# Optimization experiments

Hardware: AMD Instinct MI355X
Metric: run time of the kernel (lower is better)

Reference implementation:

```python
import jax, jax.numpy as jnp
import numpy as np

V, E, H, L = 32000, 512, 512, 2


def _cell(x, h, c, Wih, Whh, bih, bhh):
    # PyTorch LSTM cell, gate order i,f,g,o
    g = x @ Wih.T + bih + h @ Whh.T + bhh
    i, f, gg, o = jnp.split(g, 4, axis=-1)
    c = jax.nn.sigmoid(f) * c + jax.nn.sigmoid(i) * jnp.tanh(gg)
    h = jax.nn.sigmoid(o) * jnp.tanh(c)
    return h, c


def _run_layer(x, p):
    # x: [B, S, in], scan over time
    B = x.shape[0]
    h0 = jnp.zeros((B, H), x.dtype)

    def step(carry, xt):
        h, c = carry
        h, c = _cell(xt, h, c, *p)
        return (h, c), h

    (hT, cT), hs = jax.lax.scan(step, (h0, h0), jnp.swapaxes(x, 0, 1))
    return jnp.swapaxes(hs, 0, 1), hT, cT


def _forward(xs, ys, emb, enc_p, dec_p, attn_W, comb_W):
    # ---- Encoder (2-layer unidirectional LSTM) ----
    x = emb[xs]                      # [B, Senc, E]
    hs, cs = [], []
    for l in range(L):
        x, hT, cT = _run_layer(x, enc_p[l])
        hs.append(hT)
        cs.append(cT)
    enc_out = x                      # [B, Senc, H] (top layer)
    h = jnp.stack(hs)                # [L, B, H]
    c = jnp.stack(cs)
    neg = (1.0 - (xs > 0).astype(enc_out.dtype)) * 1e20  # [B, Senc]
    emb_out = jax.lax.stop_gradient(emb)  # shared output weight is detached

    # ---- Decoder: per-timestep pre-attention ('general') + LSTM ----
    def step(carry, yt):
        h, c = carry
        xe = emb[yt]                              # [B, E]
        hid = h[-1] @ attn_W.T                    # [B, H]
        pw = jnp.einsum('bh,bsh->bs', hid, enc_out) - neg
        aw = jax.nn.softmax(pw, axis=1)
        ctx = jnp.einsum('bs,bsh->bh', aw, enc_out)
        inp = jnp.tanh(jnp.concatenate([xe, ctx], axis=1) @ comb_W.T)  # [B, E]
        nh, nc = [], []
        for l in range(L):
            hl, cl = _cell(inp, h[l], c[l], *dec_p[l])
            nh.append(hl)
            nc.append(cl)
            inp = hl
        sc = inp @ emb_out.T                      # [B, V] (o2e is identity, e2s shared)
        return (jnp.stack(nh), jnp.stack(nc)), sc

    _, scores = jax.lax.scan(step, (h, c), jnp.swapaxes(ys, 0, 1))
    return jnp.swapaxes(scores, 0, 1)             # [B, Sdec, V]


def setup_inputs() -> dict:
    key = jax.random.key(0)
    B, Senc, Sdec = 32, 64, 32
    d = {}
    d['xs'] = jax.random.randint(jax.random.fold_in(key, 0), (B, Senc), 1, V)
    d['ys'] = jax.random.randint(jax.random.fold_in(key, 1), (B, Sdec), 1, V)
    d['emb'] = jax.random.normal(jax.random.fold_in(key, 2), (V, E), dtype=jnp.float32) * 0.02
    s = float(1.0 / np.sqrt(H))
    i = 3
    for pre in ('enc', 'dec'):
        for l in range(L):
            ind = E if l == 0 else H
            for name, shape in ((pre + '_Wih' + str(l), (4 * H, ind)),
                                (pre + '_Whh' + str(l), (4 * H, H)),
                                (pre + '_bih' + str(l), (4 * H,)),
                                (pre + '_bhh' + str(l), (4 * H,))):
                d[name] = jax.random.uniform(jax.random.fold_in(key, i), shape, minval=-s, maxval=s)
                i += 1
    d['attn_W'] = jax.random.uniform(jax.random.fold_in(key, i), (H, H), minval=-s, maxval=s)
    d['comb_W'] = jax.random.uniform(jax.random.fold_in(key, i + 1), (E, H + E), minval=-s, maxval=s)
    return d


def reference(xs, ys, emb,
              enc_Wih0, enc_Whh0, enc_bih0, enc_bhh0,
              enc_Wih1, enc_Whh1, enc_bih1, enc_bhh1,
              dec_Wih0, dec_Whh0, dec_bih0, dec_bhh0,
              dec_Wih1, dec_Whh1, dec_bih1, dec_bhh1,
              attn_W, comb_W):
    enc_p = [(enc_Wih0, enc_Whh0, enc_bih0, enc_bhh0),
             (enc_Wih1, enc_Whh1, enc_bih1, enc_bhh1)]
    dec_p = [(dec_Wih0, dec_Whh0, dec_bih0, dec_bhh0),
             (dec_Wih1, dec_Whh1, dec_bih1, dec_bhh1)]
    scores = _forward(xs, ys, emb, enc_p, dec_p, attn_W, comb_W)
    preds = jnp.argmax(scores[..., 1:], axis=-1) + 1   # skip padding idx 0
    return preds, scores
```

## Files before the change

kernel.cpp:

```cpp
#include <hip/hip_runtime.h>
#include <math.h>

#define B 32
#define SENC 64
#define SDEC 32
#define HDIM 512
#define EDIM 512
#define VDIM 32000
#define G4 2048
#define BH (B*HDIM)
#define NBLK 256

__device__ __forceinline__ void agent_st(float* p, float v)
{
    __hip_atomic_store(p, v, __ATOMIC_RELAXED, __HIP_MEMORY_SCOPE_AGENT);
}
__device__ __forceinline__ float4 agent_ld4(const float* p)
{
    float4 v;
    asm volatile("global_load_dwordx4 %0, %1, off sc0 sc1"
                 : "=v"(v) : "v"(p) : "memory");
    return v;
}
__device__ __forceinline__ void agent_stu(unsigned* p, unsigned v)
{
    asm volatile("global_store_dword %0, %1, off sc0 sc1"
                 :: "v"(p), "v"(v) : "memory");
}
__device__ __forceinline__ unsigned agent_ldu(const unsigned* p)
{
    unsigned v;
    asm volatile("global_load_dword %0, %1, off sc0 sc1"
                 : "=v"(v) : "v"(p) : "memory");
    asm volatile("s_waitcnt vmcnt(0)" ::: "memory");
    return v;
}

#define BF_BLK(b)  ((b) << 4)
#define BF_XD(x)   (4096 + ((x) << 4))
#define BF_RL(x)   (4224 + ((x) << 4))

__device__ __forceinline__ void grid_barrier_f(unsigned* bar, int blk, int xcd,
                                               unsigned ep)
{
    asm volatile("s_waitcnt vmcnt(0) lgkmcnt(0)" ::: "memory");
    __syncthreads();
    int tid = threadIdx.x;
    if (tid < 64) {
        if (tid == 0) agent_stu(bar + BF_BLK(blk), ep);
        if (blk < 8) {
            const unsigned* fp = bar + BF_BLK(xcd + ((tid & 31) << 3));
            for (;;) {
                unsigned v = agent_ldu(fp);
                if (__all(v >= ep)) break;
                __builtin_amdgcn_s_sleep(1);
            }
            if (tid == 0) agent_stu(bar + BF_XD(xcd), ep);
            if (blk == 0) {
                const unsigned* gp = bar + BF_XD(tid & 7);
                for (;;) {
                    unsigned v = agent_ldu(gp);
                    if (__all(v >= ep)) break;
                    __builtin_amdgcn_s_sleep(1);
                }
                if (tid < 8) agent_stu(bar + BF_RL(tid), ep);
            }
        }
        if (blk != 0) {
            const unsigned* rp = bar + BF_RL(xcd);
            for (;;) {
                unsigned v = agent_ldu(rp);
                if (__all(v >= ep)) break;
                __builtin_amdgcn_s_sleep(1);
            }
        }
    }
    __syncthreads();
}

__global__ __launch_bounds__(128) void embed_kernel(const int* __restrict__ toks,
                                                    const float* __restrict__ emb,
                                                    float* __restrict__ out)
{
    int t = blockIdx.x;
    int id = toks[t];
    const float4* src = (const float4*)(emb + (size_t)id * EDIM);
    float4* dst = (float4*)(out + (size_t)t * EDIM);
    dst[threadIdx.x] = src[threadIdx.x];
}

__global__ __launch_bounds__(256) void gemm_nt128(const float* __restrict__ A,
                                                  const float* __restrict__ Bm,
                                                  float* __restrict__ C,
                                                  const float* __restrict__ bias0,
                                                  const float* __restrict__ bias1,
                                                  int M, int N, int K, int ldb)
{
    __shared__ float As[16][128];
    __shared__ float Bs[16][128];
    int tid = threadIdx.x;
    int tx = tid & 15, ty = tid >> 4;
    int m0 = blockIdx.y * 128, n0 = blockIdx.x * 128;

    float acc[8][8];
    #pragma unroll
    for (int i = 0; i < 8; i++)
        #pragma unroll
        for (int j = 0; j < 8; j++) acc[i][j] = 0.f;

    int lr = tid >> 1, lk = (tid & 1) * 8;
    const float* Aptr = A + (size_t)(m0 + lr) * K + lk;
    const float* Bptr = Bm + (size_t)(n0 + lr) * ldb + lk;

    for (int k0 = 0; k0 < K; k0 += 16) {
        float4 a1 = *(const float4*)(Aptr + k0);
        float4 a2 = *(const float4*)(Aptr + k0 + 4);
        float4 b1 = *(const float4*)(Bptr + k0);
        float4 b2 = *(const float4*)(Bptr + k0 + 4);
        As[lk + 0][lr] = a1.x; As[lk + 1][lr] = a1.y;
        As[lk + 2][lr] = a1.z; As[lk + 3][lr] = a1.w;
        As[lk + 4][lr] = a2.x; As[lk + 5][lr] = a2.y;
        As[lk + 6][lr] = a2.z; As[lk + 7][lr] = a2.w;
        Bs[lk + 0][lr] = b1.x; Bs[lk + 1][lr] = b1.y;
        Bs[lk + 2][lr] = b1.z; Bs[lk + 3][lr] = b1.w;
        Bs[lk + 4][lr] = b2.x; Bs[lk + 5][lr] = b2.y;
        Bs[lk + 6][lr] = b2.z; Bs[lk + 7][lr] = b2.w;
        __syncthreads();
        #pragma unroll
        for (int kk = 0; kk < 16; kk++) {
            float4 av1 = *(const float4*)&As[kk][ty * 8];
            float4 av2 = *(const float4*)&As[kk][ty * 8 + 4];
            float4 bv1 = *(const float4*)&Bs[kk][tx * 8];
            float4 bv2 = *(const float4*)&Bs[kk][tx * 8 + 4];
            float am[8] = {av1.x, av1.y, av1.z, av1.w, av2.x, av2.y, av2.z, av2.w};
            float bn[8] = {bv1.x, bv1.y, bv1.z, bv1.w, bv2.x, bv2.y, bv2.z, bv2.w};
            #pragma unroll
            for (int i = 0; i < 8; i++)
                #pragma unroll
                for (int j = 0; j < 8; j++)
                    acc[i][j] += am[i] * bn[j];
        }
        __syncthreads();
    }

    int nc = n0 + tx * 8;
    float bb[8];
    #pragma unroll
    for (int j = 0; j < 8; j++) {
        bb[j] = 0.f;
        if (bias0) bb[j] += bias0[nc + j];
        if (bias1) bb[j] += bias1[nc + j];
    }
    #pragma unroll
    for (int i = 0; i < 8; i++) {
        int row = m0 + ty * 8 + i;
        float4 o1 = make_float4(acc[i][0] + bb[0], acc[i][1] + bb[1],
                                acc[i][2] + bb[2], acc[i][3] + bb[3]);
        float4 o2 = make_float4(acc[i][4] + bb[4], acc[i][5] + bb[5],
                                acc[i][6] + bb[6], acc[i][7] + bb[7]);
        *(float4*)(C + (size_t)row * N + nc) = o1;
        *(float4*)(C + (size_t)row * N + nc + 4) = o2;
    }
}

__global__ __launch_bounds__(256) void gemm_nn128(const float* __restrict__ A,
                                                  const float* __restrict__ Bm,
                                                  float* __restrict__ C,
                                                  int M, int N, int K)
{
    __shared__ float As[16][128];
    __shared__ float Bs[16][128];
    int tid = threadIdx.x;
    int tx = tid & 15, ty = tid >> 4;
    int m0 = blockIdx.y * 128, n0 = blockIdx.x * 128;

    float acc[8][8];
    #pragma unroll
    for (int i = 0; i < 8; i++)
        #pragma unroll
        for (int j = 0; j < 8; j++) acc[i][j] = 0.f;

    int lr = tid >> 1, lk = (tid & 1) * 8;
    const float* Aptr = A + (size_t)(m0 + lr) * K + lk;
    int bk = tid >> 5;
    int bn = (tid & 31) << 2;

    for (int k0 = 0; k0 < K; k0 += 16) {
        float4 a1 = *(const float4*)(Aptr + k0);
        float4 a2 = *(const float4*)(Aptr + k0 + 4);
        float4 v1 = *(const float4*)(Bm + (size_t)(k0 + bk) * N + n0 + bn);
        float4 v2 = *(const float4*)(Bm + (size_t)(k0 + bk + 8) * N + n0 + bn);
        As[lk + 0][lr] = a1.x; As[lk + 1][lr] = a1.y;
        As[lk + 2][lr] = a1.z; As[lk + 3][lr] = a1.w;
        As[lk + 4][lr] = a2.x; As[lk + 5][lr] = a2.y;
        As[lk + 6][lr] = a2.z; As[lk + 7][lr] = a2.w;
        *(float4*)&Bs[bk][bn] = v1;
        *(float4*)&Bs[bk + 8][bn] = v2;
        __syncthreads();
        #pragma unroll
        for (int kk = 0; kk < 16; kk++) {
            float4 av1 = *(const float4*)&As[kk][ty * 8];
            float4 av2 = *(const float4*)&As[kk][ty * 8 + 4];
            float4 bv1 = *(const float4*)&Bs[kk][tx * 8];
            float4 bv2 = *(const float4*)&Bs[kk][tx * 8 + 4];
            float am[8] = {av1.x, av1.y, av1.z, av1.w, av2.x, av2.y, av2.z, av2.w};
            float bv[8] = {bv1.x, bv1.y, bv1.z, bv1.w, bv2.x, bv2.y, bv2.z, bv2.w};
            #pragma unroll
            for (int i = 0; i < 8; i++)
                #pragma unroll
                for (int j = 0; j < 8; j++)
                    acc[i][j] += am[i] * bv[j];
        }
        __syncthreads();
    }

    int nc = n0 + tx * 8;
    #pragma unroll
    for (int i = 0; i < 8; i++) {
        int row = m0 + ty * 8 + i;
        float4 o1 = make_float4(acc[i][0], acc[i][1], acc[i][2], acc[i][3]);
        float4 o2 = make_float4(acc[i][4], acc[i][5], acc[i][6], acc[i][7]);
        *(float4*)(C + (size_t)row * N + nc) = o1;
        *(float4*)(C + (size_t)row * N + nc + 4) = o2;
    }
}

__device__ __forceinline__ float allreduce64(float v)
{
    #pragma unroll
    for (int m = 1; m < 64; m <<= 1) v += __shfl_xor(v, m);
    return v;
}

__device__ __forceinline__ float2 lstm_update(float i_, float f_, float g_,
                                              float o_, float c)
{
    float ig = 1.f / (1.f + expf(-i_));
    float fg = 1.f / (1.f + expf(-f_));
    float gg = tanhf(g_);
    float og = 1.f / (1.f + expf(-o_));
    float cn = fg * c + ig * gg;
    float hn = og * tanhf(cn);
    return make_float2(hn, cn);
}

__global__ __launch_bounds__(256) void enc_fused(
    const float* __restrict__ xg, const float* __restrict__ Whh0,
    const float* __restrict__ Wih1, const float* __restrict__ Whh1,
    const float* __restrict__ bih1, const float* __restrict__ bhh1,
    float* __restrict__ l1out, float* __restrict__ h0buf,
    float* __restrict__ h1buf, float* __restrict__ hT, float* __restrict__ cT,
    unsigned* __restrict__ bar)
{
    __shared__ __align__(16) float hs[16][520];
    __shared__ __align__(16) float is_[16][520];
    __shared__ float gacc[8][16][5];
    int blk = blockIdx.x;
    int xcd = blk & 7, slot = blk >> 3;
    int role = slot >> 4;
    int s2 = slot & 15;
    int jgroup = xcd * 8 + (s2 >> 1);
    int bg2 = s2 & 1;
    int tid = threadIdx.x;
    int r = tid >> 3, bb = tid & 7;
    int g = r >> 3, jj = r & 7;
    int row = (g << 9) + (jgroup << 3) + jj;
    int b0 = (bg2 << 4) + bb;
    const float* w0 = role ? (Wih1 + (size_t)row * 512)
                           : (Whh0 + (size_t)row * 512);
    const float* w1 = role ? (Whh1 + (size_t)row * 512) : (const float*)0;
    float bsum = role ? (bih1[row] + bhh1[row]) : 0.f;
    float creg = 0.f;
    unsigned ep = 0;
    int p = 0;
    for (int u = 0; u <= SENC; ++u) {
        int active = role ? (u >= 1) : (u < SENC);
        int t = role ? (u - 1) : u;
        if (active) {
            if (!role) {
                if (t == 0) {
                    float4 z = make_float4(0.f, 0.f, 0.f, 0.f);
                    #pragma unroll
                    for (int v = 0; v < 8; v++) {
                        int d = (tid + (v << 8)) << 2;
                        *(float4*)&hs[d >> 9][d & 511] = z;
                    }
                } else {
                    const float4* s4 = (const float4*)(h0buf + p * BH + ((bg2 << 4) << 9));
                    float4 hv[8];
                    #pragma unroll
                    for (int v = 0; v < 8; v++)
                        hv[v] = agent_ld4((const float*)(s4 + tid + (v << 8)));
                    asm volatile("s_waitcnt vmcnt(0)" ::: "memory");
                    #pragma unroll
                    for (int v = 0; v < 8; v++) {
                        int d = (tid + (v << 8)) << 2;
                        *(float4*)&hs[d >> 9][d & 511] = hv[v];
                    }
                }
            } else {
                const float4* s40 = (const float4*)(h0buf + p * BH + ((bg2 << 4) << 9));
                float4 hv[8];
                #pragma unroll
                for (int v = 0; v < 8; v++)
                    hv[v] = agent_ld4((const float*)(s40 + tid + (v << 8)));
                if (t == 0) {
                    asm volatile("s_waitcnt vmcnt(0)" ::: "memory");
                    float4 z = make_float4(0.f, 0.f, 0.f, 0.f);
                    #pragma unroll
                    for (int v = 0; v < 8; v++) {
                        int d = (tid + (v << 8)) << 2;
                        *(float4*)&hs[d >> 9][d & 511] = hv[v];
                        *(float4*)&is_[d >> 9][d & 511] = z;
                    }
                } else {
                    const float4* s41 = (const float4*)(h1buf + p * BH + ((bg2 << 4) << 9));
                    float4 iv[8];
                    #pragma unroll
                    for (int v = 0; v < 8; v++)
                        iv[v] = agent_ld4((const float*)(s41 + tid + (v << 8)));
                    asm volatile("s_waitcnt vmcnt(0)" ::: "memory");
                    #pragma unroll
                    for (int v = 0; v < 8; v++) {
                        int d = (tid + (v << 8)) << 2;
                        *(float4*)&hs[d >> 9][d & 511] = hv[v];
                        *(float4*)&is_[d >> 9][d & 511] = iv[v];
                    }
                }
            }
            __syncthreads();
            float acc0, acc1;
            if (!role) {
                acc0 = xg[(size_t)(b0 * SENC + t) * G4 + row];
                acc1 = xg[(size_t)((b0 + 8) * SENC + t) * G4 + row];
                float a00 = 0, a01 = 0, a02 = 0, a03 = 0;
                float a10 = 0, a11 = 0, a12 = 0, a13 = 0;
                const float* ha = hs[bb];
                const float* hb = hs[bb + 8];
                #pragma unroll 4
                for (int k = 0; k < 512; k += 4) {
                    float4 w = *(const float4*)(w0 + k);
                    float4 x = *(const float4*)(ha + k);
                    float4 y = *(const float4*)(hb + k);
                    a00 += w.x * x.x; a01 += w.y * x.y;
                    a02 += w.z * x.z; a03 += w.w * x.w;
                    a10 += w.x * y.x; a11 += w.y * y.y;
                    a12 += w.z * y.z; a13 += w.w * y.w;
                }
                acc0 += (a00 + a01) + (a02 + a03);
                acc1 += (a10 + a11) + (a12 + a13);
            } else {
                float a00 = 0, a01 = 0, a02 = 0, a03 = 0;
                float a10 = 0, a11 = 0, a12 = 0, a13 = 0;
                const float* h0a = hs[bb];
                const float* h0b = hs[bb + 8];
                const float* h1a = is_[bb];
                const float* h1b = is_[bb + 8];
                #pragma unroll 2
                for (int k = 0; k < 512; k += 4) {
                    float4 wi = *(const float4*)(w0 + k);
                    float4 wh = *(const float4*)(w1 + k);
                    float4 xa = *(const float4*)(h0a + k);
                    float4 xb = *(const float4*)(h0b + k);
                    float4 ya = *(const float4*)(h1a + k);
                    float4 yb = *(const float4*)(h1b + k);
                    a00 += wi.x * xa.x + wh.x * ya.x;
                    a01 += wi.y * xa.y + wh.y * ya.y;
                    a02 += wi.z * xa.z + wh.z * ya.z;
                    a03 += wi.w * xa.w + wh.w * ya.w;
                    a10 += wi.x * xb.x + wh.x * yb.x;
                    a11 += wi.y * xb.y + wh.y * yb.y;
                    a12 += wi.z * xb.z + wh.z * yb.z;
                    a13 += wi.w * xb.w + wh.w * yb.w;
                }
                acc0 = bsum + (a00 + a01) + (a02 + a03);
                acc1 = bsum + (a10 + a11) + (a12 + a13);
            }
            gacc[jj][bb][g] = acc0;
            gacc[jj][bb + 8][g] = acc1;
            __syncthreads();
            if (tid < 128) {
                int ujj = tid & 7, ulb = tid >> 3;
                float g0 = gacc[ujj][ulb][0], g1 = gacc[ujj][ulb][1];
                float g2 = gacc[ujj][ulb][2], g3 = gacc[ujj][ulb][3];
                float2 hc = lstm_update(g0, g1, g2, g3, creg);
                creg = hc.y;
                int ub = (bg2 << 4) + ulb;
                int ujh = (jgroup << 3) + ujj;
                if (!role) {
                    agent_st(h0buf + (p ^ 1) * BH + ub * 512 + ujh, hc.x);
                    if (t == SENC - 1) {
                        hT[ub * 512 + ujh] = hc.x;
                        cT[ub * 512 + ujh] = hc.y;
                    }
                } else {
                    agent_st(h1buf + (p ^ 1) * BH + ub * 512 + ujh, hc.x);
                    l1out[(size_t)(ub * SENC + t) * 512 + ujh] = hc.x;
                    if (t == SENC - 1) {
                        hT[BH + ub * 512 + ujh] = hc.x;
                        cT[BH + ub * 512 + ujh] = hc.y;
                    }
                }
            }
        }
        ep++;
        grid_barrier_f(bar, blk, xcd, ep);
        p ^= 1;
    }
}

__device__ __forceinline__ void cell_phase(
    const float* __restrict__ Wih, const float* __restrict__ Whh,
    float bsum,
    const float* __restrict__ inp, const float* __restrict__ h_in,
    float* __restrict__ h_out, float* __restrict__ seqout,
    float& creg, int t, int jg, int bg, int row,
    float (*hs)[520], float (*is_)[520], float (*gacc)[8][5])
{
    int tid = threadIdx.x;
    {
        const float4* hsrc4 = (const float4*)(h_in + ((bg << 3) << 9));
        const float4* isrc4 = (const float4*)(inp + ((bg << 3) << 9));
        float4 hv4[4], iv4[4];
        #pragma unroll
        for (int u = 0; u < 4; u++) {
            hv4[u] = agent_ld4((const float*)(hsrc4 + tid + (u << 8)));
            iv4[u] = agent_ld4((const float*)(isrc4 + tid + (u << 8)));
        }
        asm volatile("s_waitcnt vmcnt(0)" ::: "memory");
        #pragma unroll
        for (int u = 0; u < 4; u++) {
            int d = (tid + (u << 8)) << 2;
            int rb = d >> 9, kk = d & 511;
            *(float4*)&hs[rb][kk] = hv4[u];
            *(float4*)&is_[rb][kk] = iv4[u];
        }
    }
    __syncthreads();
    int r = tid >> 3, bb = tid & 7;
    int g = r >> 3, jj = r & 7;
    const float* wi = Wih + (size_t)row * 512;
    const float* wh = Whh + (size_t)row * 512;
    const float* ir = is_[bb];
    const float* hr = hs[bb];
    float a0 = 0.f, a1 = 0.f, a2 = 0.f, a3 = 0.f;
    #pragma unroll 8
    for (int k = 0; k < 512; k += 4) {
        float4 wiv = *(const float4*)(wi + k);
        float4 iv = *(const float4*)(ir + k);
        float4 whv = *(const float4*)(wh + k);
        float4 hv = *(const float4*)(hr + k);
        a0 += wiv.x * iv.x + whv.x * hv.x;
        a1 += wiv.y * iv.y + whv.y * hv.y;
        a2 += wiv.z * iv.z + whv.z * hv.z;
        a3 += wiv.w * iv.w + whv.w * hv.w;
    }
    gacc[jj][bb][g] = bsum + (a0 + a1) + (a2 + a3);
    __syncthreads();
    if (tid < 64) {
        int ujj = tid & 7, ubb = tid >> 3;
        float g0 = gacc[ujj][ubb][0], g1 = gacc[ujj][ubb][1];
        float g2 = gacc[ujj][ubb][2], g3 = gacc[ujj][ubb][3];
        float2 hc = lstm_update(g0, g1, g2, g3, creg);
        creg = hc.y;
        int ub = (bg << 3) + ubb, ujh = (jg << 3) + ujj;
        agent_st(h_out + ub * 512 + ujh, hc.x);
        if (seqout) seqout[(size_t)(ub * SDEC + t) * 512 + ujh] = hc.x;
    }
}

__global__ __launch_bounds__(256) void decoder_persist(
    const int* __restrict__ xs,
    const float* __restrict__ encT, const float* __restrict__ encC,
    const float* __restrict__ yg,
    const float* __restrict__ Wih0, const float* __restrict__ Whh0,
    const float* __restrict__ bih0, const float* __restrict__ bhh0,
    const float* __restrict__ Wih1, const float* __restrict__ Whh1,
    const float* __restrict__ bih1, const float* __restrict__ bhh1,
    const float* __restrict__ hT0, const float* __restrict__ cT0,
    const float* __restrict__ hT1, const float* __restrict__ cT1,
    float* __restrict__ dhb0, float* __restrict__ dhb1,
    float* __restrict__ inpbuf, float* __restrict__ h2seq,
    unsigned* __restrict__ bar)
{
    __shared__ __align__(16) float hs[8][520];
    __shared__ __align__(16) float is_[8][520];
    __shared__ float gacc[8][8][5];
    __shared__ __align__(16) float h2s[512];
    __shared__ float psum[4][64];
    __shared__ float pw[64];
    __shared__ float aw[64];
    int blk = blockIdx.x;
    int xcd = blk & 7, slot = blk >> 3;
    int jg = xcd * 8 + (slot >> 2), bg = slot & 3;
    int ab = xcd * 4 + (slot >> 3);
    int e0 = (slot & 7) << 6;
    int tid = threadIdx.x;
    int lane = tid & 63, wv = tid >> 6;
    int r = tid >> 3;
    int g = r >> 3, jj = r & 7;
    int row = (g << 9) + (jg << 3) + jj;
    float bsum0 = bih0[row] + bhh0[row];
    float bsum1 = bih1[row] + bhh1[row];
    float c0 = 0.f, c1 = 0.f;
    if (tid < 64) {
        int ujj = tid & 7, ubb = tid >> 3;
        int ub = (bg << 3) + ubb, ujh = (jg << 3) + ujj;
        c0 = cT0[ub * 512 + ujh];
        c1 = cT1[ub * 512 + ujh];
    }
    unsigned ep = 0;
    int p = 0;
    for (int t = 0; t < SDEC; ++t) {
        int q = p ^ 1;
        {
            const float* h2p = ((t == 0) ? hT1 : dhb1 + p * BH) + ab * 512;
            if (tid < 128) {
                float4 v = agent_ld4((const float*)((const float4*)h2p + tid));
                asm volatile("s_waitcnt vmcnt(0)" ::: "memory");
                ((float4*)h2s)[tid] = v;
            }
            __syncthreads();
            for (int s = wv; s < SENC; s += 4) {
                const float* rowp = encT + (size_t)(ab * SENC + s) * 512;
                float pp = 0.f;
                #pragma unroll
                for (int i = 0; i < 8; i++)
                    pp += h2s[lane + 64 * i] * rowp[lane + 64 * i];
                pp = allreduce64(pp);
                if (lane == 0)
                    pw[s] = pp - ((xs[ab * SENC + s] > 0) ? 0.f : 1e20f);
            }
            __syncthreads();
            if (tid < 64) {
                float v = pw[tid];
                float m = v;
                #pragma unroll
                for (int o = 1; o < 64; o <<= 1) m = fmaxf(m, __shfl_xor(m, o));
                float ex = expf(v - m);
                float sm = ex;
                #pragma unroll
                for (int o = 1; o < 64; o <<= 1) sm += __shfl_xor(sm, o);
                aw[tid] = ex / sm;
            }
            __syncthreads();
            {
                float part = 0.f;
                const float* cb = encC + (size_t)(ab * SENC + (wv << 4)) * 512
                                + e0 + lane;
                #pragma unroll
                for (int si = 0; si < 16; si++)
                    part += aw[(wv << 4) + si] * cb[si * 512];
                psum[wv][lane] = part;
            }
            __syncthreads();
            if (tid < 64) {
                float v = psum[0][tid] + psum[1][tid] + psum[2][tid] + psum[3][tid];
                float rr = tanhf(yg[(size_t)(ab * SDEC + t) * 512 + e0 + tid] + v);
                agent_st(inpbuf + ab * 512 + e0 + tid, rr);
            }
        }
        ep++; grid_barrier_f(bar, blk, xcd, ep);
        cell_phase(Wih0, Whh0, bsum0, inpbuf,
                   (t == 0) ? hT0 : dhb0 + p * BH, dhb0 + q * BH,
                   (float*)nullptr, c0, t, jg, bg, row, hs, is_, gacc);
        ep++; grid_barrier_f(bar, blk, xcd, ep);
        cell_phase(Wih1, Whh1, bsum1, dhb0 + q * BH,
                   (t == 0) ? hT1 : dhb1 + p * BH, dhb1 + q * BH,
                   h2seq, c1, t, jg, bg, row, hs, is_, gacc);
        ep++; grid_barrier_f(bar, blk, xcd, ep);
        p = q;
    }
}

__global__ __launch_bounds__(256) void argmax_kernel(const float* __restrict__ scores,
                                                     float* __restrict__ preds)
{
    __shared__ float sv[256];
    __shared__ int si[256];
    int m = blockIdx.x;
    const float* row = scores + (size_t)m * VDIM;
    float best = -3.4e38f;
    int bi = 0x7fffffff;
    for (int v = 1 + (int)threadIdx.x; v < VDIM; v += 256) {
        float val = row[v];
        if (val > best) { best = val; bi = v; }
    }
    sv[threadIdx.x] = best;
    si[threadIdx.x] = bi;
    __syncthreads();
    for (int s = 128; s > 0; s >>= 1) {
        if ((int)threadIdx.x < s) {
            float ov = sv[threadIdx.x + s];
            int oi = si[threadIdx.x + s];
            if (ov > sv[threadIdx.x] ||
                (ov == sv[threadIdx.x] && oi < si[threadIdx.x])) {
                sv[threadIdx.x] = ov;
                si[threadIdx.x] = oi;
            }
        }
        __syncthreads();
    }
    if (threadIdx.x == 0) preds[m] = (float)si[0];
}

extern "C" void kernel_launch(void* const* d_in, const int* in_sizes, int n_in,
                              void* d_out, int out_size, void* d_ws, size_t ws_size,
                              hipStream_t stream)
{
    const int* xs = (const int*)d_in[0];
    const int* ys = (const int*)d_in[1];
    const float* emb = (const float*)d_in[2];
    const float* W[16];
    for (int i = 0; i < 16; i++) W[i] = (const float*)d_in[3 + i];
    const float* attn_W = (const float*)d_in[19];
    const float* comb_W = (const float*)d_in[20];
    float* out = (float*)d_out;
    float* ws = (float*)d_ws;

    float* xemb   = ws;
    float* xg     = xemb + 1048576;
    float* l1out  = xg + 4194304;
    float* encT   = l1out + 1048576;
    float* h0buf  = encT + 1048576;
    float* h1buf  = h0buf + 2 * BH;
    float* hT     = h1buf + 2 * BH;
    float* cT     = hT + 2 * BH;
    unsigned* barcnt = (unsigned*)(cT + 2 * BH);
    float* yemb   = xemb;
    float* h2seq  = xg;
    float* inpbuf = xg + 524288;
    float* dhb0   = inpbuf + BH;
    float* dhb1   = dhb0 + 2 * BH;
    float* yg     = dhb1 + 2 * BH;
    float* encC   = yg + 524288;

    hipMemsetAsync(barcnt, 0, 2 * 8192 * 4, stream);

    embed_kernel<<<B * SENC, 128, 0, stream>>>(xs, emb, xemb);
    gemm_nt128<<<dim3(G4 / 128, (B * SENC) / 128), 256, 0, stream>>>(
        xemb, W[0], xg, W[2], W[3], B * SENC, G4, 512, 512);
    embed_kernel<<<B * SDEC, 128, 0, stream>>>(ys, emb, yemb);
    {
        const float* xgp = xg;
        const float* whh0 = W[1];
        const float* wih1 = W[4];
        const float* whh1 = W[5];
        const float* bih1 = W[6];
        const float* bhh1 = W[7];
        float* l1o = l1out;
        float* h0b = h0buf;
        float* h1b = h1buf;
        float* hTp = hT;
        float* cTp = cT;
        unsigned* bp = barcnt;
        void* eargs[] = {(void*)&xgp, (void*)&whh0, (void*)&wih1, (void*)&whh1,
                         (void*)&bih1, (void*)&bhh1, (void*)&l1o, (void*)&h0b,
                         (void*)&h1b, (void*)&hTp, (void*)&cTp, (void*)&bp};
        hipLaunchCooperativeKernel((void*)enc_fused, dim3(NBLK), dim3(256),
                                   eargs, 0, stream);
    }

    gemm_nn128<<<dim3(512 / 128, (B * SENC) / 128), 256, 0, stream>>>(
        l1out, attn_W, encT, B * SENC, 512, 512);
    gemm_nt128<<<dim3(512 / 128, (B * SDEC) / 128), 256, 0, stream>>>(
        yemb, comb_W, yg, nullptr, nullptr, B * SDEC, 512, 512, 1024);
    gemm_nt128<<<dim3(512 / 128, (B * SENC) / 128), 256, 0, stream>>>(
        l1out, comb_W + 512, encC, nullptr, nullptr, B * SENC, 512, 512, 1024);

    {
        const int* xs_ = xs;
        const float* encT_ = encT;
        const float* encC_ = encC;
        const float* yg_ = yg;
        const float* wih0 = W[8];
        const float* whh0 = W[9];
        const float* bih0 = W[10];
        const float* bhh0 = W[11];
        const float* wih1 = W[12];
        const float* whh1 = W[13];
        const float* bih1 = W[14];
        const float* bhh1 = W[15];
        const float* hT0_ = hT;
        const float* cT0_ = cT;
        const float* hT1_ = hT + BH;
        const float* cT1_ = cT + BH;
        float* dhb0_ = dhb0;
        float* dhb1_ = dhb1;
        float* inp_ = inpbuf;
        float* h2seq_ = h2seq;
        unsigned* bp = barcnt + 8192;
        void* dargs[] = {(void*)&xs_, (void*)&encT_, (void*)&encC_,
                         (void*)&yg_,
                         (void*)&wih0, (void*)&whh0, (void*)&bih0, (void*)&bhh0,
                         (void*)&wih1, (void*)&whh1, (void*)&bih1, (void*)&bhh1,
                         (void*)&hT0_, (void*)&cT0_, (void*)&hT1_, (void*)&cT1_,
                         (void*)&dhb0_, (void*)&dhb1_, (void*)&inp_, (void*)&h2seq_,
                         (void*)&bp};
        hipLaunchCooperativeKernel((void*)decoder_persist, dim3(NBLK), dim3(256),
                                   dargs, 0, stream);
    }

    gemm_nt128<<<dim3(VDIM / 128, (B * SDEC) / 128), 256, 0, stream>>>(
        h2seq, emb, out + B * SDEC, nullptr, nullptr, B * SDEC, VDIM, 512, 512);
    argmax_kernel<<<B * SDEC, 256, 0, stream>>>(out + B * SDEC, out);
}
```

Baseline: 3.551 ms.

## Replace grid barriers with per-block dependency flags in encoder and decoder

Removes the hierarchical grid-wide barrier in both persistent kernels. Each block now publishes an epoch flag after writing its slice and polls only the flags of the producers it depends on. In the encoder, layer-0 and layer-1 blocks run as separate loops, each waiting only on its own h inputs, so they can drift apart in a wavefront pipeline. The decoder gets three flag arrays, one per phase. This cuts barrier latency and serialization, but needs careful reasoning about double-buffer reuse (write-after-read hazards) and flag memory ordering.

```diff
diff --git a/kernel.cpp b/kernel.cpp
--- a/kernel.cpp
+++ b/kernel.cpp
@@ -36,47 +36,23 @@
     return v;
 }
 
-#define BF_BLK(b)  ((b) << 4)
-#define BF_XD(x)   (4096 + ((x) << 4))
-#define BF_RL(x)   (4224 + ((x) << 4))
-
-__device__ __forceinline__ void grid_barrier_f(unsigned* bar, int blk, int xcd,
-                                               unsigned ep)
+__device__ __forceinline__ void pollge(const unsigned* p, unsigned ep)
+{
+    for (;;) {
+        unsigned v = agent_ldu(p);
+        if (__all(v >= ep)) break;
+        __builtin_amdgcn_s_sleep(1);
+    }
+}
+
+__device__ __forceinline__ void flag_release(unsigned* line, unsigned ep)
 {
     asm volatile("s_waitcnt vmcnt(0) lgkmcnt(0)" ::: "memory");
     __syncthreads();
-    int tid = threadIdx.x;
-    if (tid < 64) {
-        if (tid == 0) agent_stu(bar + BF_BLK(blk), ep);
-        if (blk < 8) {
-            const unsigned* fp = bar + BF_BLK(xcd + ((tid & 31) << 3));
-            for (;;) {
-                unsigned v = agent_ldu(fp);
-                if (__all(v >= ep)) break;
-                __builtin_amdgcn_s_sleep(1);
-            }
-            if (tid == 0) agent_stu(bar + BF_XD(xcd), ep);
-            if (blk == 0) {
-                const unsigned* gp = bar + BF_XD(tid & 7);
-                for (;;) {
-                    unsigned v = agent_ldu(gp);
-                    if (__all(v >= ep)) break;
-                    __builtin_amdgcn_s_sleep(1);
-                }
-                if (tid < 8) agent_stu(bar + BF_RL(tid), ep);
-            }
-        }
-        if (blk != 0) {
-            const unsigned* rp = bar + BF_RL(xcd);
-            for (;;) {
-                unsigned v = agent_ldu(rp);
-                if (__all(v >= ep)) break;
-                __builtin_amdgcn_s_sleep(1);
-            }
-        }
-    }
-    __syncthreads();
-}
+    if (threadIdx.x == 0) agent_stu(line, ep);
+}
+
+#define FLG_BYTES 65536
 
 __global__ __launch_bounds__(128) void embed_kernel(const int* __restrict__ toks,
                                                     const float* __restrict__ emb,
@@ -250,11 +226,13 @@
     const float* __restrict__ bih1, const float* __restrict__ bhh1,
     float* __restrict__ l1out, float* __restrict__ h0buf,
     float* __restrict__ h1buf, float* __restrict__ hT, float* __restrict__ cT,
-    unsigned* __restrict__ bar)
+    unsigned* __restrict__ flg)
 {
     __shared__ __align__(16) float hs[16][520];
     __shared__ __align__(16) float is_[16][520];
     __shared__ float gacc[8][16][5];
+    unsigned* F0 = flg;
+    unsigned* F1 = flg + 2048;
     int blk = blockIdx.x;
     int xcd = blk & 7, slot = blk >> 3;
     int role = slot >> 4;
@@ -266,73 +244,42 @@
     int g = r >> 3, jj = r & 7;
     int row = (g << 9) + (jgroup << 3) + jj;
     int b0 = (bg2 << 4) + bb;
-    const float* w0 = role ? (Wih1 + (size_t)row * 512)
-                           : (Whh0 + (size_t)row * 512);
-    const float* w1 = role ? (Whh1 + (size_t)row * 512) : (const float*)0;
-    float bsum = role ? (bih1[row] + bhh1[row]) : 0.f;
+    unsigned* myflag = (role ? F1 : F0) + (((jgroup << 1) + bg2) << 4);
     float creg = 0.f;
-    unsigned ep = 0;
-    int p = 0;
-    for (int u = 0; u <= SENC; ++u) {
-        int active = role ? (u >= 1) : (u < SENC);
-        int t = role ? (u - 1) : u;
-        if (active) {
-            if (!role) {
-                if (t == 0) {
-                    float4 z = make_float4(0.f, 0.f, 0.f, 0.f);
-                    #pragma unroll
-                    for (int v = 0; v < 8; v++) {
-                        int d = (tid + (v << 8)) << 2;
-                        *(float4*)&hs[d >> 9][d & 511] = z;
-                    }
-                } else {
-                    const float4* s4 = (const float4*)(h0buf + p * BH + ((bg2 << 4) << 9));
-                    float4 hv[8];
-                    #pragma unroll
-                    for (int v = 0; v < 8; v++)
-                        hv[v] = agent_ld4((const float*)(s4 + tid + (v << 8)));
-                    asm volatile("s_waitcnt vmcnt(0)" ::: "memory");
-                    #pragma unroll
-                    for (int v = 0; v < 8; v++) {
-                        int d = (tid + (v << 8)) << 2;
-                        *(float4*)&hs[d >> 9][d & 511] = hv[v];
-                    }
+
+    if (!role) {
+        const float* w0 = Whh0 + (size_t)row * 512;
+        for (int t = 0; t < SENC; ++t) {
+            int ws = t & 1, rs = ws ^ 1;
+            if (t > 0 && tid < 64)
+                pollge(F0 + (((tid << 1) + bg2) << 4), (unsigned)t);
+            else if (t >= 2 && tid >= 64 && tid < 128)
+                pollge(F1 + ((((tid - 64) << 1) + bg2) << 4), (unsigned)(t - 1));
+            __syncthreads();
+            if (t == 0) {
+                float4 z = make_float4(0.f, 0.f, 0.f, 0.f);
+                #pragma unroll
+                for (int v = 0; v < 8; v++) {
+                    int d = (tid + (v << 8)) << 2;
+                    *(float4*)&hs[d >> 9][d & 511] = z;
                 }
             } else {
-                const float4* s40 = (const float4*)(h0buf + p * BH + ((bg2 << 4) << 9));
+                const float4* s4 = (const float4*)(h0buf + rs * BH + ((bg2 << 4) << 9));
                 float4 hv[8];
                 #pragma unroll
                 for (int v = 0; v < 8; v++)
-                    hv[v] = agent_ld4((const float*)(s40 + tid + (v << 8)));
-                if (t == 0) {
-                    asm volatile("s_waitcnt vmcnt(0)" ::: "memory");
-                    float4 z = make_float4(0.f, 0.f, 0.f, 0.f);
-                    #pragma unroll
-                    for (int v = 0; v < 8; v++) {
-                        int d = (tid + (v << 8)) << 2;
-                        *(float4*)&hs[d >> 9][d & 511] = hv[v];
-                        *(float4*)&is_[d >> 9][d & 511] = z;
-                    }
-                } else {
-                    const float4* s41 = (const float4*)(h1buf + p * BH + ((bg2 << 4) << 9));
-                    float4 iv[8];
-                    #pragma unroll
-                    for (int v = 0; v < 8; v++)
-                        iv[v] = agent_ld4((const float*)(s41 + tid + (v << 8)));
-                    asm volatile("s_waitcnt vmcnt(0)" ::: "memory");
-                    #pragma unroll
-                    for (int v = 0; v < 8; v++) {
-                        int d = (tid + (v << 8)) << 2;
-                        *(float4*)&hs[d >> 9][d & 511] = hv[v];
-                        *(float4*)&is_[d >> 9][d & 511] = iv[v];
-                    }
+                    hv[v] = agent_ld4((const float*)(s4 + tid + (v << 8)));
+                asm volatile("s_waitcnt vmcnt(0)" ::: "memory");
+                #pragma unroll
+                for (int v = 0; v < 8; v++) {
+                    int d = (tid + (v << 8)) << 2;
+                    *(float4*)&hs[d >> 9][d & 511] = hv[v];
                 }
             }
             __syncthreads();
-            float acc0, acc1;
-            if (!role) {
-                acc0 = xg[(size_t)(b0 * SENC + t) * G4 + row];
-                acc1 = xg[(size_t)((b0 + 8) * SENC + t) * G4 + row];
+            float acc0 = xg[(size_t)(b0 * SENC + t) * G4 + row];
+            float acc1 = xg[(size_t)((b0 + 8) * SENC + t) * G4 + row];
+            {
                 float a00 = 0, a01 = 0, a02 = 0, a03 = 0;
                 float a10 = 0, a11 = 0, a12 = 0, a13 = 0;
                 const float* ha = hs[bb];
@@ -349,7 +296,70 @@
                 }
                 acc0 += (a00 + a01) + (a02 + a03);
                 acc1 += (a10 + a11) + (a12 + a13);
-            } else {
+            }
+            gacc[jj][bb][g] = acc0;
+            gacc[jj][bb + 8][g] = acc1;
+            __syncthreads();
+            if (tid < 128) {
+                int ujj = tid & 7, ulb = tid >> 3;
+                float g0 = gacc[ujj][ulb][0], g1 = gacc[ujj][ulb][1];
+                float g2 = gacc[ujj][ulb][2], g3 = gacc[ujj][ulb][3];
+                float2 hc = lstm_update(g0, g1, g2, g3, creg);
+                creg = hc.y;
+                int ub = (bg2 << 4) + ulb;
+                int ujh = (jgroup << 3) + ujj;
+                agent_st(h0buf + ws * BH + ub * 512 + ujh, hc.x);
+                if (t == SENC - 1) {
+                    hT[ub * 512 + ujh] = hc.x;
+                    cT[ub * 512 + ujh] = hc.y;
+                }
+            }
+            flag_release(myflag, (unsigned)(t + 1));
+        }
+    } else {
+        const float* w0 = Wih1 + (size_t)row * 512;
+        const float* w1 = Whh1 + (size_t)row * 512;
+        float bsum = bih1[row] + bhh1[row];
+        for (int t = 0; t < SENC; ++t) {
+            int ws = t & 1, rs = ws ^ 1;
+            if (tid < 64)
+                pollge(F0 + (((tid << 1) + bg2) << 4), (unsigned)(t + 1));
+            else if (t > 0 && tid < 128)
+                pollge(F1 + ((((tid - 64) << 1) + bg2) << 4), (unsigned)t);
+            __syncthreads();
+            {
+                const float4* s40 = (const float4*)(h0buf + ws * BH + ((bg2 << 4) << 9));
+                float4 hv[8];
+                #pragma unroll
+                for (int v = 0; v < 8; v++)
+                    hv[v] = agent_ld4((const float*)(s40 + tid + (v << 8)));
+                if (t == 0) {
+                    asm volatile("s_waitcnt vmcnt(0)" ::: "memory");
+                    float4 z = make_float4(0.f, 0.f, 0.f, 0.f);
+                    #pragma unroll
+                    for (int v = 0; v < 8; v++) {
+                        int d = (tid + (v << 8)) << 2;
+                        *(float4*)&hs[d >> 9][d & 511] = hv[v];
+                        *(float4*)&is_[d >> 9][d & 511] = z;
+                    }
+                } else {
+                    const float4* s41 = (const float4*)(h1buf + rs * BH + ((bg2 << 4) << 9));
+                    float4 iv[8];
+                    #pragma unroll
+                    for (int v = 0; v < 8; v++)
+                        iv[v] = agent_ld4((const float*)(s41 + tid + (v << 8)));
+                    asm volatile("s_waitcnt vmcnt(0)" ::: "memory");
+                    #pragma unroll
+                    for (int v = 0; v < 8; v++) {
+                        int d = (tid + (v << 8)) << 2;
+                        *(float4*)&hs[d >> 9][d & 511] = hv[v];
+                        *(float4*)&is_[d >> 9][d & 511] = iv[v];
+                    }
+                }
+            }
+            __syncthreads();
+            float acc0, acc1;
+            {
                 float a00 = 0, a01 = 0, a02 = 0, a03 = 0;
                 float a10 = 0, a11 = 0, a12 = 0, a13 = 0;
                 const float* h0a = hs[bb];
@@ -387,25 +397,15 @@
                 creg = hc.y;
                 int ub = (bg2 << 4) + ulb;
                 int ujh = (jgroup << 3) + ujj;
-                if (!role) {
-                    agent_st(h0buf + (p ^ 1) * BH + ub * 512 + ujh, hc.x);
-                    if (t == SENC - 1) {
-                        hT[ub * 512 + ujh] = hc.x;
-                        cT[ub * 512 + ujh] = hc.y;
-                    }
-                } else {
-                    agent_st(h1buf + (p ^ 1) * BH + ub * 512 + ujh, hc.x);
-                    l1out[(size_t)(ub * SENC + t) * 512 + ujh] = hc.x;
-                    if (t == SENC - 1) {
-                        hT[BH + ub * 512 + ujh] = hc.x;
-                        cT[BH + ub * 512 + ujh] = hc.y;
-                    }
+                agent_st(h1buf + ws * BH + ub * 512 + ujh, hc.x);
+                l1out[(size_t)(ub * SENC + t) * 512 + ujh] = hc.x;
+                if (t == SENC - 1) {
+                    hT[BH + ub * 512 + ujh] = hc.x;
+                    cT[BH + ub * 512 + ujh] = hc.y;
                 }
             }
+            flag_release(myflag, (unsigned)(t + 1));
         }
-        ep++;
-        grid_barrier_f(bar, blk, xcd, ep);
-        p ^= 1;
     }
 }
 
@@ -481,7 +481,7 @@
     const float* __restrict__ hT1, const float* __restrict__ cT1,
     float* __restrict__ dhb0, float* __restrict__ dhb1,
     float* __restrict__ inpbuf, float* __restrict__ h2seq,
-    unsigned* __restrict__ bar)
+    unsigned* __restrict__ flg)
 {
     __shared__ __align__(16) float hs[8][520];
     __shared__ __align__(16) float is_[8][520];
@@ -490,11 +490,16 @@
     __shared__ float psum[4][64];
     __shared__ float pw[64];
     __shared__ float aw[64];
+    unsigned* FA = flg + 4096;
+    unsigned* FB = flg + 8192;
+    unsigned* FC = flg + 12288;
     int blk = blockIdx.x;
     int xcd = blk & 7, slot = blk >> 3;
     int jg = xcd * 8 + (slot >> 2), bg = slot & 3;
     int ab = xcd * 4 + (slot >> 3);
-    int e0 = (slot & 7) << 6;
+    int esl = slot & 7;
+    int e0 = esl << 6;
+    int abg = ab >> 3;
     int tid = threadIdx.x;
     int lane = tid & 63, wv = tid >> 6;
     int r = tid >> 3;
@@ -502,6 +507,9 @@
     int row = (g << 9) + (jg << 3) + jj;
     float bsum0 = bih0[row] + bhh0[row];
     float bsum1 = bih1[row] + bhh1[row];
+    unsigned* flagA = FA + (((ab << 3) + esl) << 4);
+    unsigned* flagB = FB + (((jg << 2) + bg) << 4);
+    unsigned* flagC = FC + (((jg << 2) + bg) << 4);
     float c0 = 0.f, c1 = 0.f;
     if (tid < 64) {
         int ujj = tid & 7, ubb = tid >> 3;
@@ -509,12 +517,13 @@
         c0 = cT0[ub * 512 + ujh];
         c1 = cT1[ub * 512 + ujh];
     }
-    unsigned ep = 0;
-    int p = 0;
     for (int t = 0; t < SDEC; ++t) {
-        int q = p ^ 1;
+        int ws = t & 1, rs = ws ^ 1;
+        if (t > 0 && tid < 64)
+            pollge(FC + (((tid << 2) + abg) << 4), (unsigned)t);
+        __syncthreads();
         {
-            const float* h2p = ((t == 0) ? hT1 : dhb1 + p * BH) + ab * 512;
+            const float* h2p = ((t == 0) ? hT1 : dhb1 + rs * BH) + ab * 512;
             if (tid < 128) {
                 float4 v = agent_ld4((const float*)((const float4*)h2p + tid));
                 asm volatile("s_waitcnt vmcnt(0)" ::: "memory");
@@ -560,16 +569,25 @@
                 agent_st(inpbuf + ab * 512 + e0 + tid, rr);
             }
         }
-        ep++; grid_barrier_f(bar, blk, xcd, ep);
+        flag_release(flagA, (unsigned)(t + 1));
+        if (tid < 64)
+            pollge(FA + (((bg << 6) + tid) << 4), (unsigned)(t + 1));
+        else if (t > 0 && tid < 128)
+            pollge(FB + ((((tid - 64) << 2) + bg) << 4), (unsigned)t);
+        __syncthreads();
         cell_phase(Wih0, Whh0, bsum0, inpbuf,
-                   (t == 0) ? hT0 : dhb0 + p * BH, dhb0 + q * BH,
+                   (t == 0) ? hT0 : dhb0 + rs * BH, dhb0 + ws * BH,
                    (float*)nullptr, c0, t, jg, bg, row, hs, is_, gacc);
-        ep++; grid_barrier_f(bar, blk, xcd, ep);
-        cell_phase(Wih1, Whh1, bsum1, dhb0 + q * BH,
-                   (t == 0) ? hT1 : dhb1 + p * BH, dhb1 + q * BH,
+        flag_release(flagB, (unsigned)(t + 1));
+        if (tid < 64)
+            pollge(FB + (((tid << 2) + bg) << 4), (unsigned)(t + 1));
+        else if (t > 0 && tid < 128)
+            pollge(FC + ((((tid - 64) << 2) + bg) << 4), (unsigned)t);
+        __syncthreads();
+        cell_phase(Wih1, Whh1, bsum1, dhb0 + ws * BH,
+                   (t == 0) ? hT1 : dhb1 + rs * BH, dhb1 + ws * BH,
                    h2seq, c1, t, jg, bg, row, hs, is_, gacc);
-        ep++; grid_barrier_f(bar, blk, xcd, ep);
-        p = q;
+        flag_release(flagC, (unsigned)(t + 1));
     }
 }
 
@@ -626,7 +644,7 @@
     float* h1buf  = h0buf + 2 * BH;
     float* hT     = h1buf + 2 * BH;
     float* cT     = hT + 2 * BH;
-    unsigned* barcnt = (unsigned*)(cT + 2 * BH);
+    unsigned* flg = (unsigned*)(cT + 2 * BH);
     float* yemb   = xemb;
     float* h2seq  = xg;
     float* inpbuf = xg + 524288;
@@ -635,7 +653,7 @@
     float* yg     = dhb1 + 2 * BH;
     float* encC   = yg + 524288;
 
-    hipMemsetAsync(barcnt, 0, 2 * 8192 * 4, stream);
+    hipMemsetAsync(flg, 0, FLG_BYTES, stream);
 
     embed_kernel<<<B * SENC, 128, 0, stream>>>(xs, emb, xemb);
     gemm_nt128<<<dim3(G4 / 128, (B * SENC) / 128), 256, 0, stream>>>(
@@ -653,10 +671,10 @@
         float* h1b = h1buf;
         float* hTp = hT;
         float* cTp = cT;
-        unsigned* bp = barcnt;
+        unsigned* fp = flg;
         void* eargs[] = {(void*)&xgp, (void*)&whh0, (void*)&wih1, (void*)&whh1,
                          (void*)&bih1, (void*)&bhh1, (void*)&l1o, (void*)&h0b,
-                         (void*)&h1b, (void*)&hTp, (void*)&cTp, (void*)&bp};
+                         (void*)&h1b, (void*)&hTp, (void*)&cTp, (void*)&fp};
         hipLaunchCooperativeKernel((void*)enc_fused, dim3(NBLK), dim3(256),
                                    eargs, 0, stream);
     }
@@ -689,14 +707,14 @@
         float* dhb1_ = dhb1;
         float* inp_ = inpbuf;
         float* h2seq_ = h2seq;
-        unsigned* bp = barcnt + 8192;
+        unsigned* fp = flg;
         void* dargs[] = {(void*)&xs_, (void*)&encT_, (void*)&encC_,
                          (void*)&yg_,
                          (void*)&wih0, (void*)&whh0, (void*)&bih0, (void*)&bhh0,
                          (void*)&wih1, (void*)&whh1, (void*)&bih1, (void*)&bhh1,
                          (void*)&hT0_, (void*)&cT0_, (void*)&hT1_, (void*)&cT1_,
                          (void*)&dhb0_, (void*)&dhb1_, (void*)&inp_, (void*)&h2seq_,
-                         (void*)&bp};
+                         (void*)&fp};
         hipLaunchCooperativeKernel((void*)decoder_persist, dim3(NBLK), dim3(256),
                                    dargs, 0, stream);
     }
```

Measured after the change: 3.152 ms. -11.2%, faster.
